# Kernel tuning notes

Hardware: AMD Instinct MI355X
Metric: run time of the kernel (lower is better)

Reference implementation:

```python
import jax, jax.numpy as jnp
import numpy as np

DIM = 512
B, S = 4, 2048


def _linear_params(key, d_in, d_out):
    kw, kb = jax.random.split(key)
    bound = 1.0 / np.sqrt(d_in)
    W = jax.random.uniform(kw, (d_out, d_in), minval=-bound, maxval=bound, dtype=jnp.float32)
    b = jax.random.uniform(kb, (d_out,), minval=-bound, maxval=bound, dtype=jnp.float32)
    return W, b


def setup_inputs() -> dict:
    key = jax.random.key(0)
    ks = jax.random.split(key, 6)
    x = jax.random.normal(ks[0], (B, S, DIM), dtype=jnp.float32)
    Wq, bq = _linear_params(ks[1], DIM, DIM)
    Wk, bk = _linear_params(ks[2], DIM, DIM)
    Wv, bv = _linear_params(ks[3], DIM, DIM)
    W1, b1 = _linear_params(ks[4], DIM, 4 * DIM)
    W2, b2 = _linear_params(ks[5], 4 * DIM, DIM)
    return {"x": x, "Wq": Wq, "bq": bq, "Wk": Wk, "bk": bk,
            "Wv": Wv, "bv": bv, "W1": W1, "b1": b1, "W2": W2, "b2": b2}


def reference(x, Wq, bq, Wk, bk, Wv, bv, W1, b1, W2, b2):
    # q, k, v projections (torch Linear: x @ W.T + b)
    q = x @ Wq.T + bq          # [B, S, D]
    k = x @ Wk.T + bk
    v = x @ Wv.T + bv
    # unscaled attention, exactly as in the source (no 1/sqrt(d))
    scores = jnp.einsum('bsd,btd->bst', q, k)   # [B, S, S]
    attn = jax.nn.softmax(scores, axis=-1) @ v  # [B, S, D]
    # 2-layer FFN with ReLU
    h = jax.nn.relu(attn @ W1.T + b1)           # [B, S, 4D]
    return h @ W2.T + b2                        # [B, S, D]
```

## Files before the change

### kernel.cpp

```cpp
#include <hip/hip_runtime.h>
#include <hip/hip_bf16.h>

typedef _Float16  f16x8  __attribute__((ext_vector_type(8)));
typedef float     f32x4  __attribute__((ext_vector_type(4)));
typedef unsigned short u16;
typedef u16       u16x4  __attribute__((ext_vector_type(4)));

__device__ __forceinline__ u16 f2h_bits(float f) {
    union { _Float16 h; u16 u; } v; v.h = (_Float16)f; return v.u;
}

__global__ __launch_bounds__(256)
void cvt_f32_f16(const float* __restrict__ X, u16* __restrict__ o, int n4) {
    const int i = blockIdx.x * 256 + threadIdx.x;
    if (i >= n4) return;
    f32x4 v = ((const f32x4*)X)[i];
    u16x4 h;
#pragma unroll
    for (int j = 0; j < 4; ++j) h[j] = f2h_bits(v[j]);
    ((u16x4*)o)[i] = h;
}

__global__ __launch_bounds__(256)
void cvt_weights(const float* __restrict__ Wq, const float* __restrict__ Wk,
                 const float* __restrict__ Wv, const float* __restrict__ W1,
                 const float* __restrict__ W2, const float* __restrict__ bq,
                 const float* __restrict__ bk,
                 u16* __restrict__ Wqk16, u16* __restrict__ Wv16,
                 u16* __restrict__ W116, u16* __restrict__ W216, float* __restrict__ bqk) {
    const int i = blockIdx.x * 256 + threadIdx.x;
    constexpr int S = 512 * 512 / 4, L = 2048 * 512 / 4;
    const float* src; u16* dst; int j;
    if      (i <     S)         { src = Wq; dst = Wqk16;           j = i;             }
    else if (i < 2 * S)         { src = Wk; dst = Wqk16 + 4 * S;   j = i - S;         }
    else if (i < 3 * S)         { src = Wv; dst = Wv16;            j = i - 2 * S;     }
    else if (i < 3 * S + L)     { src = W1; dst = W116;            j = i - 3 * S;     }
    else if (i < 3 * S + 2 * L) { src = W2; dst = W216;            j = i - 3 * S - L; }
    else if (i < 3 * S + 2 * L + 256) {
        const int g = (i - 3 * S - 2 * L) * 4;
#pragma unroll
        for (int t = 0; t < 4; ++t) bqk[g + t] = (g + t < 512) ? bq[g + t] : bk[g + t - 512];
        return;
    } else return;
    f32x4 v = ((const f32x4*)src)[j];
    u16x4 h;
#pragma unroll
    for (int t = 0; t < 4; ++t) h[t] = f2h_bits(v[t]);
    ((u16x4*)dst)[j] = h;
}

template<int ROWS>
__device__ __forceinline__ void stage_rows(const u16* __restrict__ g0, int ld, u16* lds, int wl) {
    const int l = threadIdx.x & 63;
    constexpr int CH = ROWS / 64;
#pragma unroll
    for (int i = 0; i < CH; ++i) {
        const int base = (wl * CH + i) << 10;
        const int off  = base + (l << 4);
        const int row  = off >> 6;
        const int cb   = off & 63;
        const u16* g = g0 + (size_t)row * ld + (cb >> 1);
        __builtin_amdgcn_global_load_lds((const __attribute__((address_space(1))) void*)g,
                                         (__attribute__((address_space(3))) void*)((char*)lds + base),
                                         16, 0, 0);
    }
}

template<int BN, int SPLITK, bool RELU, int OMODE, typename TC>
__global__ __launch_bounds__(256 * SPLITK, 4)
void gemm16(const u16* __restrict__ Ag, const u16* __restrict__ Bg,
            const float* __restrict__ bias, TC* __restrict__ C,
            int K, int lda, int ldb, int ldc,
            long sA, long sB, long sC)
{
    const int nx = gridDim.x, ny = gridDim.y;
    const int nwg = nx * ny * gridDim.z;
    int bid = blockIdx.x + nx * (blockIdx.y + ny * blockIdx.z);
    int swz = (bid & 7) * (nwg >> 3) + (bid >> 3);
    const int n0 = (swz % nx) * BN; swz /= nx;
    const int m0 = (swz % ny) * 128;
    const int bz = swz / ny;

    constexpr int FR = (BN == 128) ? 4 : 2;
    constexpr int ATILE = 128 * 32;
    constexpr int BTILE = BN * 32;
    constexpr int BUFSZ = ATILE + BTILE;
    __shared__ __align__(16) u16 smem[SPLITK * 2 * BUFSZ];

    const int l  = threadIdx.x & 63, w = threadIdx.x >> 6;
    const int kw = (SPLITK == 2) ? (w >> 2) : 0;
    const int wl = w & 3;
    const int wr = (BN == 128) ? (wl >> 1) * 64 : wl * 32;
    const int wc = (BN == 128) ? (wl & 1) * 64 : 0;
    const int lr = l & 15, kg = l >> 4;

    const int Kh = K / SPLITK;
    const int kb = kw * Kh;

    const u16* Ab = Ag + (size_t)bz * sA + (size_t)m0 * lda + kb;
    const u16* Bb = Bg + (size_t)bz * sB + (size_t)n0 * ldb + kb;
    C += (size_t)bz * sC;

    u16* mybuf = smem + kw * 2 * BUFSZ;

    auto stage = [&](int buf, int k0) {
        u16* s = mybuf + buf * BUFSZ;
        stage_rows<128>(Ab + k0, lda, s, wl);
        stage_rows<BN>(Bb + k0, ldb, s + ATILE, wl);
    };

    f32x4 acc[FR][4] = {};

    stage(0, 0);
    __syncthreads();
    int cur = 0;
    for (int k0 = 0; k0 < Kh; k0 += 32) {
        if (k0 + 32 < Kh) stage(cur ^ 1, k0 + 32);
        const u16* sA = mybuf + cur * BUFSZ;
        const u16* sB = sA + ATILE;

        f16x8 a[FR], b[4];
#pragma unroll
        for (int i = 0; i < FR; ++i) a[i] = *(const f16x8*)&sA[(wr + i * 16 + lr) * 32 + kg * 8];
#pragma unroll
        for (int i = 0; i < 4; ++i)  b[i] = *(const f16x8*)&sB[(wc + i * 16 + lr) * 32 + kg * 8];
#pragma unroll
        for (int mi = 0; mi < FR; ++mi)
#pragma unroll
            for (int ni = 0; ni < 4; ++ni)
                acc[mi][ni] = __builtin_amdgcn_mfma_f32_16x16x32_f16(a[mi], b[ni], acc[mi][ni], 0, 0, 0);
        __syncthreads();
        cur ^= 1;
    }

    if constexpr (SPLITK == 2) {
        float* red = (float*)smem;
        const int slot = (wl * 64 + l) * (FR * 4);
        if (kw == 1) {
#pragma unroll
            for (int mi = 0; mi < FR; ++mi)
#pragma unroll
                for (int ni = 0; ni < 4; ++ni)
                    *(f32x4*)&red[(slot + mi * 4 + ni) * 4] = acc[mi][ni];
        }
        __syncthreads();
        if (kw == 1) return;
#pragma unroll
        for (int mi = 0; mi < FR; ++mi)
#pragma unroll
            for (int ni = 0; ni < 4; ++ni)
                acc[mi][ni] += *(const f32x4*)&red[(slot + mi * 4 + ni) * 4];
    }

#pragma unroll
    for (int mi = 0; mi < FR; ++mi) {
        const int mbase = m0 + wr + mi * 16 + kg * 4;
#pragma unroll
        for (int ni = 0; ni < 4; ++ni) {
            const int n = n0 + wc + ni * 16 + lr;
            const float bv = bias ? bias[n] : 0.0f;
            if constexpr (OMODE == 3) {
                const int bb = mbase >> 11;
                const int s  = mbase & 2047;
                u16x4 o;
#pragma unroll
                for (int j = 0; j < 4; ++j) o[j] = f2h_bits(acc[mi][ni][j] + bv);
                *(u16x4*)((u16*)C + ((size_t)bb * 512 + n) * 2048 + s) = o;
            } else {
#pragma unroll
                for (int j = 0; j < 4; ++j) {
                    float x = acc[mi][ni][j] + bv;
                    if constexpr (RELU) x = fmaxf(x, 0.0f);
                    const size_t idx = (size_t)(mbase + j) * ldc + n;
                    if constexpr (OMODE == 0) C[idx] = x;
                    else                      ((u16*)C)[idx] = f2h_bits(x);
                }
            }
        }
    }
}

__global__ __launch_bounds__(256)
void softmax_rows(const float* __restrict__ S, u16* __restrict__ P) {
    const int row = blockIdx.x;
    const float* s = S + (size_t)row * 2048;
    u16* p = P + (size_t)row * 2048;
    const int t = threadIdx.x;
    const int l = t & 63, w = t >> 6;

    f32x4 v0 = *(const f32x4*)&s[t * 8];
    f32x4 v1 = *(const f32x4*)&s[t * 8 + 4];
    float m = v0[0];
#pragma unroll
    for (int j = 1; j < 4; ++j) m = fmaxf(m, v0[j]);
#pragma unroll
    for (int j = 0; j < 4; ++j) m = fmaxf(m, v1[j]);
#pragma unroll
    for (int off = 1; off < 64; off <<= 1) m = fmaxf(m, __shfl_xor(m, off));

    __shared__ float redm[4], reds[4];
    if (l == 0) redm[w] = m;
    __syncthreads();
    m = fmaxf(fmaxf(redm[0], redm[1]), fmaxf(redm[2], redm[3]));

    float e[8]; float sum = 0.0f;
#pragma unroll
    for (int j = 0; j < 4; ++j) { e[j]     = __expf(v0[j] - m); sum += e[j]; }
#pragma unroll
    for (int j = 0; j < 4; ++j) { e[4 + j] = __expf(v1[j] - m); sum += e[4 + j]; }
#pragma unroll
    for (int off = 1; off < 64; off <<= 1) sum += __shfl_xor(sum, off);
    if (l == 0) reds[w] = sum;
    __syncthreads();
    sum = reds[0] + reds[1] + reds[2] + reds[3];
    const float inv = 1.0f / sum;

    u16x4 o0, o1;
#pragma unroll
    for (int j = 0; j < 4; ++j) { o0[j] = f2h_bits(e[j] * inv); o1[j] = f2h_bits(e[4 + j] * inv); }
    *(u16x4*)&p[t * 8]     = o0;
    *(u16x4*)&p[t * 8 + 4] = o1;
}

extern "C" void kernel_launch(void* const* d_in, const int* in_sizes, int n_in,
                              void* d_out, int out_size, void* d_ws, size_t ws_size,
                              hipStream_t stream) {
    const float* x  = (const float*)d_in[0];
    const float* Wq = (const float*)d_in[1];
    const float* bq = (const float*)d_in[2];
    const float* Wk = (const float*)d_in[3];
    const float* bk = (const float*)d_in[4];
    const float* Wv = (const float*)d_in[5];
    const float* bv = (const float*)d_in[6];
    const float* W1 = (const float*)d_in[7];
    const float* b1 = (const float*)d_in[8];
    const float* W2 = (const float*)d_in[9];
    const float* b2 = (const float*)d_in[10];
    float* out = (float*)d_out;

    char* ws = (char*)d_ws;
    size_t off = 0;
    auto alloc = [&](size_t bytes) { void* p = ws + off; off += (bytes + 255) & ~(size_t)255; return p; };
    u16* x16    = (u16*)alloc(8192ull * 512 * 2);
    u16* Wqk16  = (u16*)alloc(1024ull * 512 * 2);
    u16* Wv16   = (u16*)alloc(512ull * 512 * 2);
    u16* W116   = (u16*)alloc(2048ull * 512 * 2);
    u16* W216   = (u16*)alloc(512ull * 2048 * 2);
    float* bqk  = (float*)alloc(1024 * 4);
    u16* pbuf   = (u16*)alloc(4ull * 2048 * 2048 * 2);
    u16* vt     = (u16*)alloc(4ull * 512 * 2048 * 2);
    float* scores = (float*)alloc(4ull * 2048 * 2048 * 4);
    u16* qk   = pbuf;
    u16* P    = pbuf;
    u16* attn = x16;
    u16* h    = (u16*)scores;
    if (ws_size < off) return;

    dim3 blk(256), blk2(512);

    cvt_f32_f16<<<dim3(4096), blk, 0, stream>>>(x, x16, 8192 * 512 / 4);
    cvt_weights<<<dim3(2817), blk, 0, stream>>>(Wq, Wk, Wv, W1, W2, bq, bk,
                                                Wqk16, Wv16, W116, W216, bqk);

    gemm16<64, 1, false, 2, u16><<<dim3(16, 64, 1), blk, 0, stream>>>(
        x16, Wqk16, bqk, qk, 512, 512, 512, 1024, 0, 0, 0);
    gemm16<64, 2, false, 3, u16><<<dim3(8, 64, 1), blk2, 0, stream>>>(
        x16, Wv16, bv, vt, 512, 512, 512, 0, 0, 0, 0);
    gemm16<128, 1, false, 0, float><<<dim3(16, 16, 4), blk, 0, stream>>>(
        qk, qk + 512, nullptr, scores, 512, 1024, 1024, 2048,
        2048L * 1024, 2048L * 1024, 2048L * 2048);
    softmax_rows<<<dim3(8192), blk, 0, stream>>>(scores, P);
    gemm16<64, 2, false, 2, u16><<<dim3(8, 16, 4), blk2, 0, stream>>>(
        P, vt, nullptr, attn, 2048, 2048, 2048, 512,
        2048L * 2048, 512L * 2048, 2048L * 512);
    gemm16<128, 1, true, 2, u16><<<dim3(16, 64, 1), blk, 0, stream>>>(
        attn, W116, b1, h, 512, 512, 512, 2048, 0, 0, 0);
    gemm16<64, 2, false, 0, float><<<dim3(8, 64, 1), blk2, 0, stream>>>(
        h, W216, b2, out, 2048, 2048, 2048, 512, 0, 0, 0);
}
```

Baseline: 192.1 us.

## Triple-buffer GEMM LDS staging with vmcnt waits and merge conversion kernels

Turns the GEMM main loop from double to triple buffering in LDS. Each tile is issued two iterations ahead, and explicit s_waitcnt vmcnt counts plus a raw s_barrier replace __syncthreads, so global-to-LDS loads overlap more compute. It also merges the x and weight fp32→fp16 conversion kernels into one launch, and lowers the occupancy hint for BN=128 single-split kernels to 3. The cost is 50% more LDS per block, and the hand-written vmcnt counts must exactly match the number of loads issued per stage.

```diff
diff --git a/kernel.cpp b/kernel.cpp
--- a/kernel.cpp
+++ b/kernel.cpp
@@ -10,34 +10,36 @@
     union { _Float16 h; u16 u; } v; v.h = (_Float16)f; return v.u;
 }
 
+template<int N> __device__ __forceinline__ void vmwait() {
+    if constexpr (N == 0)      asm volatile("s_waitcnt vmcnt(0)" ::: "memory");
+    else if constexpr (N == 3) asm volatile("s_waitcnt vmcnt(3)" ::: "memory");
+    else if constexpr (N == 4) asm volatile("s_waitcnt vmcnt(4)" ::: "memory");
+}
+__device__ __forceinline__ void pipe_barrier() {
+    __builtin_amdgcn_s_barrier();
+    __builtin_amdgcn_sched_barrier(0);
+}
+
 __global__ __launch_bounds__(256)
-void cvt_f32_f16(const float* __restrict__ X, u16* __restrict__ o, int n4) {
+void cvt_all(const float* __restrict__ x,
+             const float* __restrict__ Wq, const float* __restrict__ Wk,
+             const float* __restrict__ Wv, const float* __restrict__ W1,
+             const float* __restrict__ W2, const float* __restrict__ bq,
+             const float* __restrict__ bk,
+             u16* __restrict__ x16, u16* __restrict__ Wqk16, u16* __restrict__ Wv16,
+             u16* __restrict__ W116, u16* __restrict__ W216, float* __restrict__ bqk) {
     const int i = blockIdx.x * 256 + threadIdx.x;
-    if (i >= n4) return;
-    f32x4 v = ((const f32x4*)X)[i];
-    u16x4 h;
-#pragma unroll
-    for (int j = 0; j < 4; ++j) h[j] = f2h_bits(v[j]);
-    ((u16x4*)o)[i] = h;
-}
-
-__global__ __launch_bounds__(256)
-void cvt_weights(const float* __restrict__ Wq, const float* __restrict__ Wk,
-                 const float* __restrict__ Wv, const float* __restrict__ W1,
-                 const float* __restrict__ W2, const float* __restrict__ bq,
-                 const float* __restrict__ bk,
-                 u16* __restrict__ Wqk16, u16* __restrict__ Wv16,
-                 u16* __restrict__ W116, u16* __restrict__ W216, float* __restrict__ bqk) {
-    const int i = blockIdx.x * 256 + threadIdx.x;
+    constexpr int X4 = 8192 * 512 / 4;
     constexpr int S = 512 * 512 / 4, L = 2048 * 512 / 4;
     const float* src; u16* dst; int j;
-    if      (i <     S)         { src = Wq; dst = Wqk16;           j = i;             }
-    else if (i < 2 * S)         { src = Wk; dst = Wqk16 + 4 * S;   j = i - S;         }
-    else if (i < 3 * S)         { src = Wv; dst = Wv16;            j = i - 2 * S;     }
-    else if (i < 3 * S + L)     { src = W1; dst = W116;            j = i - 3 * S;     }
-    else if (i < 3 * S + 2 * L) { src = W2; dst = W216;            j = i - 3 * S - L; }
-    else if (i < 3 * S + 2 * L + 256) {
-        const int g = (i - 3 * S - 2 * L) * 4;
+    if      (i < X4)                { src = x;  dst = x16;           j = i;                }
+    else if (i < X4 + S)            { src = Wq; dst = Wqk16;         j = i - X4;           }
+    else if (i < X4 + 2 * S)        { src = Wk; dst = Wqk16 + 4 * S; j = i - X4 - S;       }
+    else if (i < X4 + 3 * S)        { src = Wv; dst = Wv16;          j = i - X4 - 2 * S;   }
+    else if (i < X4 + 3 * S + L)    { src = W1; dst = W116;          j = i - X4 - 3 * S;   }
+    else if (i < X4 + 3 * S + 2 * L){ src = W2; dst = W216;          j = i - X4 - 3 * S - L; }
+    else if (i < X4 + 3 * S + 2 * L + 256) {
+        const int g = (i - X4 - 3 * S - 2 * L) * 4;
 #pragma unroll
         for (int t = 0; t < 4; ++t) bqk[g + t] = (g + t < 512) ? bq[g + t] : bk[g + t - 512];
         return;
@@ -67,7 +69,7 @@
 }
 
 template<int BN, int SPLITK, bool RELU, int OMODE, typename TC>
-__global__ __launch_bounds__(256 * SPLITK, 4)
+__global__ __launch_bounds__(256 * SPLITK, (SPLITK == 2) ? 4 : (BN == 128 ? 3 : 4))
 void gemm16(const u16* __restrict__ Ag, const u16* __restrict__ Bg,
             const float* __restrict__ bias, TC* __restrict__ C,
             int K, int lda, int ldb, int ldc,
@@ -85,7 +87,8 @@
     constexpr int ATILE = 128 * 32;
     constexpr int BTILE = BN * 32;
     constexpr int BUFSZ = ATILE + BTILE;
-    __shared__ __align__(16) u16 smem[SPLITK * 2 * BUFSZ];
+    constexpr int LPT = 2 + BN / 64;
+    __shared__ __align__(16) u16 smem[SPLITK * 3 * BUFSZ];
 
     const int l  = threadIdx.x & 63, w = threadIdx.x >> 6;
     const int kw = (SPLITK == 2) ? (w >> 2) : 0;
@@ -96,27 +99,30 @@
 
     const int Kh = K / SPLITK;
     const int kb = kw * Kh;
+    const int T  = Kh >> 5;
 
     const u16* Ab = Ag + (size_t)bz * sA + (size_t)m0 * lda + kb;
     const u16* Bb = Bg + (size_t)bz * sB + (size_t)n0 * ldb + kb;
     C += (size_t)bz * sC;
 
-    u16* mybuf = smem + kw * 2 * BUFSZ;
-
-    auto stage = [&](int buf, int k0) {
-        u16* s = mybuf + buf * BUFSZ;
-        stage_rows<128>(Ab + k0, lda, s, wl);
-        stage_rows<BN>(Bb + k0, ldb, s + ATILE, wl);
+    u16* mybuf = smem + kw * 3 * BUFSZ;
+
+    auto stage = [&](int slot, int t) {
+        u16* s = mybuf + slot * BUFSZ;
+        stage_rows<128>(Ab + t * 32, lda, s, wl);
+        stage_rows<BN>(Bb + t * 32, ldb, s + ATILE, wl);
     };
 
     f32x4 acc[FR][4] = {};
 
     stage(0, 0);
-    __syncthreads();
-    int cur = 0;
-    for (int k0 = 0; k0 < Kh; k0 += 32) {
-        if (k0 + 32 < Kh) stage(cur ^ 1, k0 + 32);
-        const u16* sA = mybuf + cur * BUFSZ;
+    stage(1, 1);
+    vmwait<LPT>();
+    pipe_barrier();
+
+    for (int t = 0; t < T; ++t) {
+        if (t + 2 < T) stage((t + 2) % 3, t + 2);
+        const u16* sA = mybuf + (t % 3) * BUFSZ;
         const u16* sB = sA + ATILE;
 
         f16x8 a[FR], b[4];
@@ -129,8 +135,10 @@
 #pragma unroll
             for (int ni = 0; ni < 4; ++ni)
                 acc[mi][ni] = __builtin_amdgcn_mfma_f32_16x16x32_f16(a[mi], b[ni], acc[mi][ni], 0, 0, 0);
-        __syncthreads();
-        cur ^= 1;
+
+        if (t + 2 < T) vmwait<LPT>();
+        else           vmwait<0>();
+        pipe_barrier();
     }
 
     if constexpr (SPLITK == 2) {
@@ -258,9 +266,8 @@
 
     dim3 blk(256), blk2(512);
 
-    cvt_f32_f16<<<dim3(4096), blk, 0, stream>>>(x, x16, 8192 * 512 / 4);
-    cvt_weights<<<dim3(2817), blk, 0, stream>>>(Wq, Wk, Wv, W1, W2, bq, bk,
-                                                Wqk16, Wv16, W116, W216, bqk);
+    cvt_all<<<dim3(6913), blk, 0, stream>>>(x, Wq, Wk, Wv, W1, W2, bq, bk,
+                                            x16, Wqk16, Wv16, W116, W216, bqk);
 
     gemm16<64, 1, false, 2, u16><<<dim3(16, 64, 1), blk, 0, stream>>>(
         x16, Wqk16, bqk, qk, 512, 512, 512, 1024, 0, 0, 0);
```

Result: no change. 194.7 us (+1.3%).

## Store scores as fp16 offsets from per-block row max, fuse QKV and conversions

Applied to the files above, without the earlier changes.

The QK^T GEMM now writes scores as fp16 values relative to each 64-column block's row max, plus a small fp32 array of those block maxima. The softmax reads half the bytes and adds the block max back, which removes the fp32 scores round trip. The Q/K/V projections are merged into one GEMM with a split epilogue that writes V transposed, and the x and weight conversions are merged into one launch. Storing offsets from the block max limits fp16 overflow, but precision drops for large negative offsets, and the epilogue does scalar u16 stores plus shuffle reductions.

```diff
diff --git a/kernel.cpp b/kernel.cpp
--- a/kernel.cpp
+++ b/kernel.cpp
@@ -5,41 +5,40 @@
 typedef float     f32x4  __attribute__((ext_vector_type(4)));
 typedef unsigned short u16;
 typedef u16       u16x4  __attribute__((ext_vector_type(4)));
+typedef u16       u16x8  __attribute__((ext_vector_type(8)));
 
 __device__ __forceinline__ u16 f2h_bits(float f) {
     union { _Float16 h; u16 u; } v; v.h = (_Float16)f; return v.u;
 }
+__device__ __forceinline__ float h2f(u16 b) {
+    union { u16 u; _Float16 h; } v; v.u = b; return (float)v.h;
+}
 
 __global__ __launch_bounds__(256)
-void cvt_f32_f16(const float* __restrict__ X, u16* __restrict__ o, int n4) {
+void cvt_all(const float* __restrict__ x,
+             const float* __restrict__ Wq, const float* __restrict__ Wk,
+             const float* __restrict__ Wv, const float* __restrict__ W1,
+             const float* __restrict__ W2, const float* __restrict__ bq,
+             const float* __restrict__ bk, const float* __restrict__ bv,
+             u16* __restrict__ x16, u16* __restrict__ Wqkv16,
+             u16* __restrict__ W116, u16* __restrict__ W216, float* __restrict__ bqkv) {
     const int i = blockIdx.x * 256 + threadIdx.x;
-    if (i >= n4) return;
-    f32x4 v = ((const f32x4*)X)[i];
-    u16x4 h;
-#pragma unroll
-    for (int j = 0; j < 4; ++j) h[j] = f2h_bits(v[j]);
-    ((u16x4*)o)[i] = h;
-}
-
-__global__ __launch_bounds__(256)
-void cvt_weights(const float* __restrict__ Wq, const float* __restrict__ Wk,
-                 const float* __restrict__ Wv, const float* __restrict__ W1,
-                 const float* __restrict__ W2, const float* __restrict__ bq,
-                 const float* __restrict__ bk,
-                 u16* __restrict__ Wqk16, u16* __restrict__ Wv16,
-                 u16* __restrict__ W116, u16* __restrict__ W216, float* __restrict__ bqk) {
-    const int i = blockIdx.x * 256 + threadIdx.x;
+    constexpr int X4 = 8192 * 512 / 4;
     constexpr int S = 512 * 512 / 4, L = 2048 * 512 / 4;
     const float* src; u16* dst; int j;
-    if      (i <     S)         { src = Wq; dst = Wqk16;           j = i;             }
-    else if (i < 2 * S)         { src = Wk; dst = Wqk16 + 4 * S;   j = i - S;         }
-    else if (i < 3 * S)         { src = Wv; dst = Wv16;            j = i - 2 * S;     }
-    else if (i < 3 * S + L)     { src = W1; dst = W116;            j = i - 3 * S;     }
-    else if (i < 3 * S + 2 * L) { src = W2; dst = W216;            j = i - 3 * S - L; }
-    else if (i < 3 * S + 2 * L + 256) {
-        const int g = (i - 3 * S - 2 * L) * 4;
-#pragma unroll
-        for (int t = 0; t < 4; ++t) bqk[g + t] = (g + t < 512) ? bq[g + t] : bk[g + t - 512];
+    if      (i < X4)                 { src = x;  dst = x16;            j = i;                  }
+    else if (i < X4 + S)             { src = Wq; dst = Wqkv16;         j = i - X4;             }
+    else if (i < X4 + 2 * S)         { src = Wk; dst = Wqkv16 + 4 * S; j = i - X4 - S;         }
+    else if (i < X4 + 3 * S)         { src = Wv; dst = Wqkv16 + 8 * S; j = i - X4 - 2 * S;     }
+    else if (i < X4 + 3 * S + L)     { src = W1; dst = W116;           j = i - X4 - 3 * S;     }
+    else if (i < X4 + 3 * S + 2 * L) { src = W2; dst = W216;           j = i - X4 - 3 * S - L; }
+    else if (i < X4 + 3 * S + 2 * L + 384) {
+        const int g = (i - X4 - 3 * S - 2 * L) * 4;
+#pragma unroll
+        for (int t = 0; t < 4; ++t) {
+            const int e = g + t;
+            bqkv[e] = (e < 512) ? bq[e] : (e < 1024 ? bk[e - 512] : bv[e - 1024]);
+        }
         return;
     } else return;
     f32x4 v = ((const f32x4*)src)[j];
@@ -69,7 +68,7 @@
 template<int BN, int SPLITK, bool RELU, int OMODE, typename TC>
 __global__ __launch_bounds__(256 * SPLITK, 4)
 void gemm16(const u16* __restrict__ Ag, const u16* __restrict__ Bg,
-            const float* __restrict__ bias, TC* __restrict__ C,
+            const float* __restrict__ bias, TC* __restrict__ C, void* __restrict__ xtra,
             int K, int lda, int ldb, int ldc,
             long sA, long sB, long sC)
 {
@@ -152,6 +151,31 @@
                 acc[mi][ni] += *(const f32x4*)&red[(slot + mi * 4 + ni) * 4];
     }
 
+    if constexpr (OMODE == 5) {
+        float* MB = (float*)xtra + (size_t)bz * 2048 * 32;
+        const int cb = (n0 + wc) >> 6;
+#pragma unroll
+        for (int mi = 0; mi < FR; ++mi) {
+            const int mbase = m0 + wr + mi * 16 + kg * 4;
+#pragma unroll
+            for (int j = 0; j < 4; ++j) {
+                float rmax = fmaxf(fmaxf(acc[mi][0][j], acc[mi][1][j]),
+                                   fmaxf(acc[mi][2][j], acc[mi][3][j]));
+                rmax = fmaxf(rmax, __shfl_xor(rmax, 1));
+                rmax = fmaxf(rmax, __shfl_xor(rmax, 2));
+                rmax = fmaxf(rmax, __shfl_xor(rmax, 4));
+                rmax = fmaxf(rmax, __shfl_xor(rmax, 8));
+                const int row = mbase + j;
+                if ((l & 15) == 0) MB[(size_t)row * 32 + cb] = rmax;
+#pragma unroll
+                for (int ni = 0; ni < 4; ++ni)
+                    ((u16*)C)[(size_t)row * ldc + (n0 + wc + ni * 16 + lr)] =
+                        f2h_bits(acc[mi][ni][j] - rmax);
+            }
+        }
+        return;
+    }
+
 #pragma unroll
     for (int mi = 0; mi < FR; ++mi) {
         const int mbase = m0 + wr + mi * 16 + kg * 4;
@@ -159,13 +183,20 @@
         for (int ni = 0; ni < 4; ++ni) {
             const int n = n0 + wc + ni * 16 + lr;
             const float bv = bias ? bias[n] : 0.0f;
-            if constexpr (OMODE == 3) {
-                const int bb = mbase >> 11;
-                const int s  = mbase & 2047;
-                u16x4 o;
-#pragma unroll
-                for (int j = 0; j < 4; ++j) o[j] = f2h_bits(acc[mi][ni][j] + bv);
-                *(u16x4*)((u16*)C + ((size_t)bb * 512 + n) * 2048 + s) = o;
+            if constexpr (OMODE == 4) {
+                if (n0 < 1024) {
+#pragma unroll
+                    for (int j = 0; j < 4; ++j)
+                        ((u16*)C)[(size_t)(mbase + j) * ldc + n] = f2h_bits(acc[mi][ni][j] + bv);
+                } else {
+                    const int d  = n - 1024;
+                    const int bb = mbase >> 11;
+                    const int s  = mbase & 2047;
+                    u16x4 o;
+#pragma unroll
+                    for (int j = 0; j < 4; ++j) o[j] = f2h_bits(acc[mi][ni][j] + bv);
+                    *(u16x4*)((u16*)xtra + ((size_t)bb * 512 + d) * 2048 + s) = o;
+                }
             } else {
 #pragma unroll
                 for (int j = 0; j < 4; ++j) {
@@ -181,20 +212,22 @@
 }
 
 __global__ __launch_bounds__(256)
-void softmax_rows(const float* __restrict__ S, u16* __restrict__ P) {
+void softmax_rows(const u16* __restrict__ S16, const float* __restrict__ MB, u16* __restrict__ P) {
     const int row = blockIdx.x;
-    const float* s = S + (size_t)row * 2048;
+    const u16* s = S16 + (size_t)row * 2048;
     u16* p = P + (size_t)row * 2048;
     const int t = threadIdx.x;
     const int l = t & 63, w = t >> 6;
-
-    f32x4 v0 = *(const f32x4*)&s[t * 8];
-    f32x4 v1 = *(const f32x4*)&s[t * 8 + 4];
-    float m = v0[0];
-#pragma unroll
-    for (int j = 1; j < 4; ++j) m = fmaxf(m, v0[j]);
-#pragma unroll
-    for (int j = 0; j < 4; ++j) m = fmaxf(m, v1[j]);
+    const float base = MB[(size_t)row * 32 + (t >> 3)];
+
+    u16x8 hv = *(const u16x8*)&s[t * 8];
+    float v[8];
+#pragma unroll
+    for (int j = 0; j < 8; ++j) v[j] = h2f(hv[j]) + base;
+
+    float m = v[0];
+#pragma unroll
+    for (int j = 1; j < 8; ++j) m = fmaxf(m, v[j]);
 #pragma unroll
     for (int off = 1; off < 64; off <<= 1) m = fmaxf(m, __shfl_xor(m, off));
 
@@ -205,9 +238,7 @@
 
     float e[8]; float sum = 0.0f;
 #pragma unroll
-    for (int j = 0; j < 4; ++j) { e[j]     = __expf(v0[j] - m); sum += e[j]; }
-#pragma unroll
-    for (int j = 0; j < 4; ++j) { e[4 + j] = __expf(v1[j] - m); sum += e[4 + j]; }
+    for (int j = 0; j < 8; ++j) { e[j] = __expf(v[j] - m); sum += e[j]; }
 #pragma unroll
     for (int off = 1; off < 64; off <<= 1) sum += __shfl_xor(sum, off);
     if (l == 0) reds[w] = sum;
@@ -242,39 +273,36 @@
     size_t off = 0;
     auto alloc = [&](size_t bytes) { void* p = ws + off; off += (bytes + 255) & ~(size_t)255; return p; };
     u16* x16    = (u16*)alloc(8192ull * 512 * 2);
-    u16* Wqk16  = (u16*)alloc(1024ull * 512 * 2);
-    u16* Wv16   = (u16*)alloc(512ull * 512 * 2);
+    u16* Wqkv16 = (u16*)alloc(1536ull * 512 * 2);
     u16* W116   = (u16*)alloc(2048ull * 512 * 2);
     u16* W216   = (u16*)alloc(512ull * 2048 * 2);
-    float* bqk  = (float*)alloc(1024 * 4);
+    float* bqkv = (float*)alloc(1536 * 4);
     u16* pbuf   = (u16*)alloc(4ull * 2048 * 2048 * 2);
+    u16* s16    = (u16*)alloc(4ull * 2048 * 2048 * 2);
     u16* vt     = (u16*)alloc(4ull * 512 * 2048 * 2);
-    float* scores = (float*)alloc(4ull * 2048 * 2048 * 4);
+    float* mb   = (float*)alloc(8192ull * 32 * 4);
     u16* qk   = pbuf;
     u16* P    = pbuf;
     u16* attn = x16;
-    u16* h    = (u16*)scores;
+    u16* h    = s16;
     if (ws_size < off) return;
 
     dim3 blk(256), blk2(512);
 
-    cvt_f32_f16<<<dim3(4096), blk, 0, stream>>>(x, x16, 8192 * 512 / 4);
-    cvt_weights<<<dim3(2817), blk, 0, stream>>>(Wq, Wk, Wv, W1, W2, bq, bk,
-                                                Wqk16, Wv16, W116, W216, bqk);
-
-    gemm16<64, 1, false, 2, u16><<<dim3(16, 64, 1), blk, 0, stream>>>(
-        x16, Wqk16, bqk, qk, 512, 512, 512, 1024, 0, 0, 0);
-    gemm16<64, 2, false, 3, u16><<<dim3(8, 64, 1), blk2, 0, stream>>>(
-        x16, Wv16, bv, vt, 512, 512, 512, 0, 0, 0, 0);
-    gemm16<128, 1, false, 0, float><<<dim3(16, 16, 4), blk, 0, stream>>>(
-        qk, qk + 512, nullptr, scores, 512, 1024, 1024, 2048,
+    cvt_all<<<dim3(6914), blk, 0, stream>>>(x, Wq, Wk, Wv, W1, W2, bq, bk, bv,
+                                            x16, Wqkv16, W116, W216, bqkv);
+
+    gemm16<64, 1, false, 4, u16><<<dim3(24, 64, 1), blk, 0, stream>>>(
+        x16, Wqkv16, bqkv, qk, vt, 512, 512, 512, 1024, 0, 0, 0);
+    gemm16<128, 1, false, 5, u16><<<dim3(16, 16, 4), blk, 0, stream>>>(
+        qk, qk + 512, nullptr, s16, mb, 512, 1024, 1024, 2048,
         2048L * 1024, 2048L * 1024, 2048L * 2048);
-    softmax_rows<<<dim3(8192), blk, 0, stream>>>(scores, P);
+    softmax_rows<<<dim3(8192), blk, 0, stream>>>(s16, mb, P);
     gemm16<64, 2, false, 2, u16><<<dim3(8, 16, 4), blk2, 0, stream>>>(
-        P, vt, nullptr, attn, 2048, 2048, 2048, 512,
+        P, vt, nullptr, attn, nullptr, 2048, 2048, 2048, 512,
         2048L * 2048, 512L * 2048, 2048L * 512);
     gemm16<128, 1, true, 2, u16><<<dim3(16, 64, 1), blk, 0, stream>>>(
-        attn, W116, b1, h, 512, 512, 512, 2048, 0, 0, 0);
+        attn, W116, b1, h, nullptr, 512, 512, 512, 2048, 0, 0, 0);
     gemm16<64, 2, false, 0, float><<<dim3(8, 64, 1), blk2, 0, stream>>>(
-        h, W216, b2, out, 2048, 2048, 2048, 512, 0, 0, 0);
-}
+        h, W216, b2, out, nullptr, 2048, 2048, 2048, 512, 0, 0, 0);
+}
```

Result: faster. 186.0 us (-3.2%).
